# Performance work log

Hardware: AMD Instinct MI355X
Metric: run time of the kernel (lower is better)

The kernel has to match this reference:

```python
import jax, jax.numpy as jnp
import numpy as np


def conv2d(x, w, b=None):
    # NCHW conv, stride 1, 'same' padding inferred from kernel size
    ph, pw = w.shape[2] // 2, w.shape[3] // 2
    y = jax.lax.conv_general_dilated(
        x, w, window_strides=(1, 1), padding=[(ph, ph), (pw, pw)],
        dimension_numbers=('NCHW', 'OIHW', 'NCHW'))
    if b is not None:
        y = y + b[None, :, None, None]
    return y


def gelu(v):
    return jax.nn.gelu(v, approximate=False)  # torch nn.GELU default (erf)


def lrelu(v):
    return jnp.where(v >= 0, v, 0.1 * v)  # LeakyReLU(0.1)


def setup_inputs() -> dict:
    key = jax.random.key(0)
    ks = jax.random.split(key, 16)
    B, C, H, W = 2, 32, 256, 256
    s = 0.05
    return {
        'x':      jax.random.normal(ks[0], (B, C, H, W), jnp.float32),
        'key':    jax.random.normal(ks[1], (B, C, H, W), jnp.float32),
        'w_off1': jax.random.normal(ks[2], (32, 64, 3, 3), jnp.float32) * s,
        'b_off1': jax.random.normal(ks[3], (32,), jnp.float32) * s,
        'w_off2': jax.random.normal(ks[4], (32, 32, 3, 3), jnp.float32) * s,
        'b_off2': jax.random.normal(ks[5], (32,), jnp.float32) * s,
        'w_dcn':  jax.random.normal(ks[6], (288, 64, 3, 3), jnp.float32) * s,
        'b_dcn':  jax.random.normal(ks[7], (288,), jnp.float32) * s,
        'w_sel':  jax.random.normal(ks[8], (1, 3, 3, 3), jnp.float32) * s,
        'b_sel':  jax.random.normal(ks[9], (1,), jnp.float32) * s,
        'w_t1':   jax.random.normal(ks[10], (32, 32, 3, 3), jnp.float32) * s,
        'w_t2':   jax.random.normal(ks[11], (128, 32, 1, 1), jnp.float32) * s,
        'w_t3':   jax.random.normal(ks[12], (128, 128, 3, 3), jnp.float32) * s,
        'w_t4':   jax.random.normal(ks[13], (32, 128, 1, 1), jnp.float32) * s,
        'w_t5':   jax.random.normal(ks[14], (32, 32, 3, 3), jnp.float32) * s,
    }


def reference(x, key, w_off1, b_off1, w_off2, b_off2, w_dcn, b_dcn,
              w_sel, b_sel, w_t1, w_t2, w_t3, w_t4, w_t5):
    B, C, H, W = x.shape
    TOPK = 3
    # offset branch
    off = lrelu(conv2d(jnp.concatenate([x, key], axis=1), w_off1, b_off1))
    off = lrelu(conv2d(off, w_off2, b_off2))
    # dcn_attention proxy: conv over (key, offset) producing C*9 candidate warps
    warp = conv2d(jnp.concatenate([key, off], axis=1), w_dcn, b_dcn)
    warp = warp.reshape(B, C, 9, H, W)
    # correlation of each of 9 candidates with x, per pixel
    corr = jnp.einsum('bcohw,bchw->bohw', warp, x)            # [B,9,H,W]
    corr = corr.reshape(B, 9, H * W).transpose(0, 2, 1)       # [B,HW,9]
    _, idx = jax.lax.top_k(corr, TOPK)                        # [B,HW,3]
    # gather selected candidates per pixel per channel
    warp_p = warp.reshape(B, C, 9, H * W).transpose(0, 3, 2, 1)   # [B,HW,9,C]
    sel = jnp.take_along_axis(warp_p, idx[..., None], axis=2)     # [B,HW,3,C]
    key_warp = sel.reshape(B, H, W, TOPK, C).transpose(0, 4, 3, 1, 2)
    key_warp = key_warp.reshape(B * C, TOPK, H, W)
    key_warp = conv2d(key_warp, w_sel, b_sel).reshape(B, C, H, W)
    # tail: conv-GELU bottleneck stack
    y = conv2d(key_warp, w_t1)
    y = conv2d(gelu(y), w_t2)
    y = conv2d(gelu(y), w_t3)
    y = conv2d(gelu(y), w_t4)
    y = conv2d(gelu(y), w_t5)
    return y
```

## Files before the change

### kernel.cpp

```cpp
#include <hip/hip_runtime.h>
#include <math.h>

static constexpr int H = 256, W = 256, HW = H * W;

typedef __attribute__((ext_vector_type(8))) _Float16 half8v;
typedef __attribute__((ext_vector_type(4))) _Float16 half4v;
typedef __attribute__((ext_vector_type(4))) float  float4v;

__device__ __forceinline__ half8v h8zero() {
  half8v z;
  #pragma unroll
  for (int i = 0; i < 8; ++i) z[i] = (_Float16)0;
  return z;
}

__device__ __forceinline__ float gelu_f(float v) {
  return 0.5f * v * (1.0f + erff(v * 0.70710678118654752440f));
}
template<int ACT>
__device__ __forceinline__ float apply_act(float v) {
  if constexpr (ACT == 1) return v >= 0.f ? v : 0.1f * v;
  if constexpr (ACT == 2) return gelu_f(v);
  return v;
}

__global__ __launch_bounds__(256)
void pack2_k(const float* __restrict__ inA, _Float16* __restrict__ hiA, _Float16* __restrict__ loA,
             const float* __restrict__ inB, _Float16* __restrict__ hiB, _Float16* __restrict__ loB)
{
  const int p = blockIdx.x * 256 + threadIdx.x;
  const int b = blockIdx.y;
  const float* in = blockIdx.z ? inB : inA;
  _Float16* hi = blockIdx.z ? hiB : hiA;
  _Float16* lo = blockIdx.z ? loB : loA;
  const float* ip = in + (size_t)b * 32 * HW + p;
  __attribute__((aligned(16))) _Float16 hv[32], lv[32];
  #pragma unroll
  for (int c = 0; c < 32; ++c) {
    float v = ip[(size_t)c * HW];
    _Float16 h = (_Float16)v;
    hv[c] = h;
    lv[c] = (_Float16)((v - (float)h) * 2048.0f);
  }
  size_t ob = ((size_t)b * HW + p) * 32;
  #pragma unroll
  for (int j = 0; j < 4; ++j) {
    *(half8v*)&hi[ob + j * 8] = *(half8v*)&hv[j * 8];
    *(half8v*)&lo[ob + j * 8] = *(half8v*)&lv[j * 8];
  }
}

__device__ __forceinline__ void prep_w_body(const float* w, _Float16* hi, _Float16* lo,
                                            int OC, int CIN, int tid)
{
  if (tid >= OC * CIN * 9) return;
  int ci = tid % CIN; int r = tid / CIN; int oc = r % OC; int tap = r / OC;
  float v = w[((size_t)oc * CIN + ci) * 9 + tap];
  _Float16 h = (_Float16)v;
  hi[tid] = h;
  lo[tid] = (_Float16)((v - (float)h) * 2048.0f);
}
__global__ __launch_bounds__(256)
void prep3_w_k(const float* __restrict__ w0, _Float16* __restrict__ h0, _Float16* __restrict__ l0, int OC0, int CIN0, int nb0,
               const float* __restrict__ w1, _Float16* __restrict__ h1, _Float16* __restrict__ l1, int OC1, int CIN1, int nb1,
               const float* __restrict__ w2, _Float16* __restrict__ h2, _Float16* __restrict__ l2, int OC2, int CIN2)
{
  int bb = blockIdx.x;
  if (bb < nb0)            prep_w_body(w0, h0, l0, OC0, CIN0, bb * 256 + threadIdx.x);
  else if (bb < nb0 + nb1) prep_w_body(w1, h1, l1, OC1, CIN1, (bb - nb0) * 256 + threadIdx.x);
  else                     prep_w_body(w2, h2, l2, OC2, CIN2, (bb - nb0 - nb1) * 256 + threadIdx.x);
}

template<int CIN, int OC, int OCB, int ACT, int OMODE, int SPLIT>
__global__ __launch_bounds__(256)
void conv3x3_mfma_k(const _Float16* __restrict__ iH0, const _Float16* __restrict__ iL0,
                    const _Float16* __restrict__ iH1, const _Float16* __restrict__ iL1, int cin0,
                    const _Float16* __restrict__ wHi, const _Float16* __restrict__ wLo,
                    const float* __restrict__ bias,
                    float* __restrict__ outF, _Float16* __restrict__ oH, _Float16* __restrict__ oL)
{
  constexpr int NOF  = OCB / 16;
  constexpr int NAQ  = (SPLIT == 3) ? NOF : 1;
  constexpr int REC  = (SPLIT == 3) ? 64 : 32;
  constexpr int nOcg = OC / OCB;
  __shared__ _Float16 sB[6 * 66 * REC];

  const int l  = threadIdx.x & 63;
  const int wv = threadIdx.x >> 6;

  const int bid = blockIdx.x;
  const int xcd = bid & 7, q = bid >> 3;
  const int ocg  = q % nOcg;
  const int tIdx = (q / nOcg) * 8 + xcd;
  const int b   = tIdx >> 8;
  const int x0  = ((tIdx >> 6) & 3) * 64;
  const int y0  = (tIdx & 63) * 4;
  const int oc0 = ocg * OCB;

  float4v accP[NOF][4];
  float4v accQ[NAQ][4];
  #pragma unroll
  for (int j = 0; j < NOF; ++j)
    #pragma unroll
    for (int f = 0; f < 4; ++f)
      accP[j][f] = (float4v){0.f, 0.f, 0.f, 0.f};
  #pragma unroll
  for (int j = 0; j < NAQ; ++j)
    #pragma unroll
    for (int f = 0; f < 4; ++f)
      accQ[j][f] = (float4v){0.f, 0.f, 0.f, 0.f};

  const int k8  = (l >> 4) * 8;
  const int ocl = l & 15;
  const int rowy = y0 + wv;
  const int sq  = l & 3;
  const int spx = l >> 2;

  #pragma unroll 1
  for (int cc = 0; cc < CIN; cc += 32) {
    const _Float16 *cbH, *cbL;
    if (cc < cin0) {
      size_t o = (size_t)(b * (cin0 >> 5) + (cc >> 5)) * HW * 32;
      cbH = iH0 + o; cbL = iL0 + o;
    } else {
      size_t o = (size_t)(b * ((CIN - cin0) >> 5) + ((cc - cin0) >> 5)) * HW * 32;
      cbH = iH1 + o; cbL = iL1 + o;
    }
    __syncthreads();
    if constexpr (SPLIT == 3) {
      #pragma unroll 2
      for (int t = wv; t < 60; t += 4) {
        int r = t / 10; int rem = t - r * 10; int bsel = rem / 5; int s = rem - bsel * 5;
        const _Float16* src = bsel ? cbL : cbH;
        int gy = y0 + r - 1;
        bool vy = (gy >= 0) && (gy < H);
        int gyc = gy < 0 ? 0 : (gy >= H ? H - 1 : gy);
        int pxl = s * 16 + spx;
        bool lact = (s < 4) || (l < 8);
        int gx = x0 + pxl - 1;
        bool vx = (gx >= 0) && (gx < W);
        int gxc = gx < 0 ? 0 : (gx >= W ? W - 1 : gx);
        half8v v = h8zero();
        if (lact && vy && vx)
          v = *(const half8v*)&src[((size_t)gyc * W + gxc) * 32 + sq * 8];
        int cls = (sq + (bsel ? 4 : 0)) ^ (pxl & 7);
        if (lact)
          *(half8v*)&sB[(r * 66 + pxl) * 64 + cls * 8] = v;
      }
    } else {
      #pragma unroll 2
      for (int t = wv; t < 30; t += 4) {
        int r = t / 5; int s = t - r * 5;
        int gy = y0 + r - 1;
        bool vy = (gy >= 0) && (gy < H);
        int gyc = gy < 0 ? 0 : (gy >= H ? H - 1 : gy);
        int pxl = s * 16 + spx;
        bool lact = (s < 4) || (l < 8);
        int gx = x0 + pxl - 1;
        bool vx = (gx >= 0) && (gx < W);
        int gxc = gx < 0 ? 0 : (gx >= W ? W - 1 : gx);
        half8v v = h8zero();
        if (lact && vy && vx)
          v = *(const half8v*)&cbH[((size_t)gyc * W + gxc) * 32 + sq * 8];
        int cls = (sq ^ pxl) & 3;
        if (lact)
          *(half8v*)&sB[(r * 66 + pxl) * 32 + cls * 8] = v;
      }
    }
    __syncthreads();

    #pragma unroll 1
    for (int tap = 0; tap < 9; ++tap) {
      const int dy = tap / 3, dx = tap - 3 * (tap / 3);
      half8v ah[NOF], aq[NAQ];
      const _Float16* hp = wHi + ((size_t)tap * OC + oc0 + ocl) * CIN + cc + k8;
      #pragma unroll
      for (int j = 0; j < NOF; ++j)
        ah[j] = *(const half8v*)(hp + (size_t)j * 16 * CIN);
      if constexpr (SPLIT == 3) {
        const _Float16* lp = wLo + ((size_t)tap * OC + oc0 + ocl) * CIN + cc + k8;
        #pragma unroll
        for (int j = 0; j < NOF; ++j)
          aq[j] = *(const half8v*)(lp + (size_t)j * 16 * CIN);
      }
      const int px = ocl + dx;
      if constexpr (SPLIT == 3) {
        const int rbase = ((wv + dy) * 66 + px) * 64;
        const int clsH = (l >> 4) ^ (px & 7);
        const int clsQ = ((l >> 4) + 4) ^ (px & 7);
        __builtin_amdgcn_s_setprio(1);
        #pragma unroll
        for (int f = 0; f < 4; ++f) {
          half8v bh = *(const half8v*)&sB[rbase + f * 1024 + clsH * 8];
          half8v bq = *(const half8v*)&sB[rbase + f * 1024 + clsQ * 8];
          #pragma unroll
          for (int j = 0; j < NOF; ++j) {
            accP[j][f] = __builtin_amdgcn_mfma_f32_16x16x32_f16(ah[j], bh, accP[j][f], 0, 0, 0);
            accQ[j][f] = __builtin_amdgcn_mfma_f32_16x16x32_f16(ah[j], bq, accQ[j][f], 0, 0, 0);
            accQ[j][f] = __builtin_amdgcn_mfma_f32_16x16x32_f16(aq[j], bh, accQ[j][f], 0, 0, 0);
          }
        }
        __builtin_amdgcn_s_setprio(0);
      } else {
        const int rbase = ((wv + dy) * 66 + px) * 32;
        const int clsH = ((l >> 4) ^ px) & 3;
        __builtin_amdgcn_s_setprio(1);
        #pragma unroll
        for (int f = 0; f < 4; ++f) {
          half8v bh = *(const half8v*)&sB[rbase + f * 512 + clsH * 8];
          #pragma unroll
          for (int j = 0; j < NOF; ++j)
            accP[j][f] = __builtin_amdgcn_mfma_f32_16x16x32_f16(ah[j], bh, accP[j][f], 0, 0, 0);
        }
        __builtin_amdgcn_s_setprio(0);
      }
    }
  }

  #pragma unroll
  for (int j = 0; j < NOF; ++j)
    #pragma unroll
    for (int f = 0; f < 4; ++f) {
      const int px  = x0 + f * 16 + ocl;
      const int occ = oc0 + j * 16 + (l >> 4) * 4;
      float vv4[4];
      #pragma unroll
      for (int r = 0; r < 4; ++r) {
        float bv = bias ? bias[occ + r] : 0.f;
        float vv = accP[j][f][r] + bv;
        if constexpr (SPLIT == 3) vv += accQ[j][f][r] * (1.0f / 2048.0f);
        vv4[r] = apply_act<ACT>(vv);
      }
      if constexpr (OMODE == 0) {
        #pragma unroll
        for (int r = 0; r < 4; ++r)
          outF[((size_t)(b * OC + occ + r) * H + rowy) * W + px] = vv4[r];
      } else if constexpr (OMODE == 1) {
        __attribute__((aligned(8))) _Float16 hv[4], lv[4];
        #pragma unroll
        for (int r = 0; r < 4; ++r) {
          _Float16 h = (_Float16)vv4[r];
          hv[r] = h;
          lv[r] = (_Float16)((vv4[r] - (float)h) * 2048.0f);
        }
        size_t ob = ((size_t)b * HW + (size_t)rowy * W + px) * OC + occ;
        *(half4v*)&oH[ob] = *(half4v*)&hv[0];
        *(half4v*)&oL[ob] = *(half4v*)&lv[0];
      } else {
        __attribute__((aligned(8))) _Float16 hv[4];
        #pragma unroll
        for (int r = 0; r < 4; ++r) hv[r] = (_Float16)vv4[r];
        size_t ob = ((size_t)b * HW + (size_t)rowy * W + px) * OC + occ;
        *(half4v*)&oH[ob] = *(half4v*)&hv[0];
      }
    }
}

template<int CIN, int OCB, int ACT>
__global__ __launch_bounds__(256)
void conv1x1_nhwc_k(const _Float16* __restrict__ in, const float* __restrict__ w,
                    _Float16* __restrict__ oH, int OC)
{
  __shared__ __align__(16) float sW[OCB][CIN];
  const int b   = blockIdx.y;
  const int oc0 = blockIdx.z * OCB;
  for (int t = threadIdx.x; t < OCB * CIN; t += 256)
    sW[t / CIN][t % CIN] = w[(size_t)(oc0 + t / CIN) * CIN + (t % CIN)];
  __syncthreads();

  const int pb = blockIdx.x * 1024 + threadIdx.x;
  float acc[OCB][4];
  #pragma unroll
  for (int o = 0; o < OCB; ++o)
    #pragma unroll
    for (int i = 0; i < 4; ++i) acc[o][i] = 0.f;

  #pragma unroll 1
  for (int c0 = 0; c0 < CIN; c0 += 8) {
    float v[4][8];
    #pragma unroll
    for (int i = 0; i < 4; ++i) {
      const _Float16* ip = in + ((size_t)b * HW + pb + i * 256) * CIN + c0;
      half8v hv8 = *(const half8v*)ip;
      #pragma unroll
      for (int j = 0; j < 8; ++j) v[i][j] = (float)hv8[j];
    }
    #pragma unroll
    for (int o = 0; o < OCB; ++o) {
      const float4 w0 = *(const float4*)&sW[o][c0];
      const float4 w1 = *(const float4*)&sW[o][c0 + 4];
      #pragma unroll
      for (int i = 0; i < 4; ++i) {
        acc[o][i] += v[i][0]*w0.x + v[i][1]*w0.y + v[i][2]*w0.z + v[i][3]*w0.w
                   + v[i][4]*w1.x + v[i][5]*w1.y + v[i][6]*w1.z + v[i][7]*w1.w;
      }
    }
  }
  #pragma unroll
  for (int i = 0; i < 4; ++i) {
    __attribute__((aligned(16))) _Float16 hv[OCB];
    #pragma unroll
    for (int o = 0; o < OCB; ++o)
      hv[o] = (_Float16)apply_act<ACT>(acc[o][i]);
    size_t ob = ((size_t)(b * (OC >> 5) + (oc0 >> 5)) * HW + pb + i * 256) * 32 + (oc0 & 31);
    #pragma unroll
    for (int j = 0; j < OCB / 8; ++j)
      *(half8v*)&oH[ob + j * 8] = *(half8v*)&hv[j * 8];
  }
}

__global__ __launch_bounds__(256)
void corr_topk_k(const float* __restrict__ warp, const float* __restrict__ x,
                 int* __restrict__ idxo)
{
  const int p2 = (blockIdx.x * 256 + threadIdx.x) * 2;
  const int b = blockIdx.y;
  float corr[9][2];
  #pragma unroll
  for (int o = 0; o < 9; ++o) { corr[o][0] = 0.f; corr[o][1] = 0.f; }
  #pragma unroll 1
  for (int c = 0; c < 32; ++c) {
    float2 xv = *(const float2*)&x[((size_t)b * 32 + c) * HW + p2];
    const float* wp = warp + ((size_t)b * 288 + (size_t)c * 9) * HW + p2;
    #pragma unroll
    for (int o = 0; o < 9; ++o) {
      float2 wv = *(const float2*)&wp[(size_t)o * HW];
      corr[o][0] += wv.x * xv.x;
      corr[o][1] += wv.y * xv.y;
    }
  }
  int2 packs;
  #pragma unroll
  for (int i = 0; i < 2; ++i) {
    unsigned mask = 0;
    int packed = 0;
    #pragma unroll
    for (int t = 0; t < 3; ++t) {
      float best = -INFINITY; int bi = 0;
      #pragma unroll
      for (int o = 0; o < 9; ++o) {
        bool take = (((mask >> o) & 1u) == 0u) && (corr[o][i] > best);
        best = take ? corr[o][i] : best;
        bi   = take ? o          : bi;
      }
      mask   |= 1u << bi;
      packed |= bi << (4 * t);
    }
    ((int*)&packs)[i] = packed;
  }
  *(int2*)&idxo[(size_t)b * HW + p2] = packs;
}

__global__ __launch_bounds__(256)
void selconv_k(const float* __restrict__ warp, const int* __restrict__ idxp,
               const float* __restrict__ wsel, const float* __restrict__ bsel,
               _Float16* __restrict__ oH)
{
  const int tx = threadIdx.x & 31, ty = threadIdx.x >> 5;
  const int px = blockIdx.x * 32 + tx;
  const int py = blockIdx.y * 8 + ty;
  const int b  = blockIdx.z;

  int  nidx[9];
  bool nval[9];
  int  qoff[9];
  #pragma unroll
  for (int kh = 0; kh < 3; ++kh)
    #pragma unroll
    for (int kw = 0; kw < 3; ++kw) {
      int k = kh * 3 + kw;
      int qy = py + kh - 1, qx = px + kw - 1;
      nval[k] = (qy >= 0 && qy < H && qx >= 0 && qx < W);
      qoff[k] = qy * W + qx;
      nidx[k] = nval[k] ? idxp[(size_t)b * HW + qoff[k]] : 0;
    }

  float ws27[27];
  #pragma unroll
  for (int i = 0; i < 27; ++i) ws27[i] = wsel[i];
  const float bs = bsel[0];

  float arr[32];
  #pragma unroll 1
  for (int c = 0; c < 32; ++c) {
    float acc = bs;
    const float* wb = warp + ((size_t)b * 288 + (size_t)c * 9) * HW;
    #pragma unroll
    for (int k = 0; k < 9; ++k) {
      if (nval[k]) {
        int pk = nidx[k];
        #pragma unroll
        for (int t = 0; t < 3; ++t) {
          int o = (pk >> (4 * t)) & 15;
          acc += ws27[t * 9 + k] * wb[(size_t)o * HW + qoff[k]];
        }
      }
    }
    arr[c] = acc;
  }

  __attribute__((aligned(16))) _Float16 hv[32];
  #pragma unroll
  for (int c = 0; c < 32; ++c) hv[c] = (_Float16)arr[c];
  size_t ob = ((size_t)b * HW + (size_t)py * W + px) * 32;
  #pragma unroll
  for (int j = 0; j < 4; ++j)
    *(half8v*)&oH[ob + j * 8] = *(half8v*)&hv[j * 8];
}

extern "C" void kernel_launch(void* const* d_in, const int* in_sizes, int n_in,
                              void* d_out, int out_size, void* d_ws, size_t ws_size,
                              hipStream_t stream) {
  const float* x      = (const float*)d_in[0];
  const float* key    = (const float*)d_in[1];
  const float* w_off1 = (const float*)d_in[2];
  const float* b_off1 = (const float*)d_in[3];
  const float* w_off2 = (const float*)d_in[4];
  const float* b_off2 = (const float*)d_in[5];
  const float* w_dcn  = (const float*)d_in[6];
  const float* b_dcn  = (const float*)d_in[7];
  const float* w_sel  = (const float*)d_in[8];
  const float* b_sel  = (const float*)d_in[9];
  const float* w_t1   = (const float*)d_in[10];
  const float* w_t2   = (const float*)d_in[11];
  const float* w_t3   = (const float*)d_in[12];
  const float* w_t4   = (const float*)d_in[13];
  const float* w_t5   = (const float*)d_in[14];

  char* ws = (char*)d_ws;
  float* warp = (float*)(ws);
  _Float16* xH  = (_Float16*)(ws);
  _Float16* xL  = (_Float16*)(ws + 8388608);
  _Float16* o1H = (_Float16*)(ws + 16777216);
  _Float16* o1L = (_Float16*)(ws + 25165824);
  _Float16* w1H = (_Float16*)(ws + 33554432);
  _Float16* w1L = w1H + 18432;
  _Float16* w2H = w1L + 18432;
  _Float16* w2L = w2H + 9216;
  _Float16* kH  = (_Float16*)(ws + 150994944);
  _Float16* kL  = (_Float16*)(ws + 159383552);
  _Float16* o2H = (_Float16*)(ws + 167772160);
  _Float16* o2L = (_Float16*)(ws + 176160768);
  _Float16* wdH = (_Float16*)(ws + 184549376);
  _Float16* wdL = wdH + 165888;
  int*      idxb = (int*)(ws + 150994944);
  _Float16* kwH  = (_Float16*)(ws + 159383552);
  _Float16* twB  = (_Float16*)(ws + 176160768);
  _Float16* t1H_w = twB;
  _Float16* t1L_w = twB + 9216;
  _Float16* t3H_w = twB + 18432;
  _Float16* t3L_w = twB + 165888;
  _Float16* t5H_w = twB + 313344;
  _Float16* t5L_w = twB + 322560;
  _Float16* y1  = (_Float16*)(ws);
  _Float16* t2H = (_Float16*)(ws + 16777216);
  _Float16* y3  = (_Float16*)(ws + 83886080);
  _Float16* t4H = (_Float16*)(ws + 50331648);
  float* out = (float*)d_out;

  dim3 blk(256);

  pack2_k<<<dim3(256, 2, 2), blk, 0, stream>>>(x, xH, xL, key, kH, kL);
  prep3_w_k<<<dim3(756), blk, 0, stream>>>(
      w_off1, w1H, w1L, 32, 64, 72,
      w_off2, w2H, w2L, 32, 32, 36,
      w_dcn,  wdH, wdL, 288, 64);

  conv3x3_mfma_k<64, 32, 32, 1, 1, 3><<<dim3(512), blk, 0, stream>>>(
      xH, xL, kH, kL, 32, w1H, w1L, b_off1, nullptr, o1H, o1L);
  conv3x3_mfma_k<32, 32, 32, 1, 1, 3><<<dim3(512), blk, 0, stream>>>(
      o1H, o1L, o1H, o1L, 32, w2H, w2L, b_off2, nullptr, o2H, o2L);
  conv3x3_mfma_k<64, 288, 32, 0, 0, 3><<<dim3(4608), blk, 0, stream>>>(
      kH, kL, o2H, o2L, 32, wdH, wdL, b_dcn, warp, nullptr, nullptr);
  corr_topk_k<<<dim3(128, 2), blk, 0, stream>>>(warp, x, idxb);
  selconv_k<<<dim3(8, 32, 2), blk, 0, stream>>>(warp, idxb, w_sel, b_sel, kwH);

  prep3_w_k<<<dim3(648), blk, 0, stream>>>(
      w_t1, t1H_w, t1L_w, 32, 32, 36,
      w_t3, t3H_w, t3L_w, 128, 128, 576,
      w_t5, t5H_w, t5L_w, 32, 32);

  conv3x3_mfma_k<32, 32, 32, 2, 3, 1><<<dim3(512), blk, 0, stream>>>(
      kwH, kwH, kwH, kwH, 32, t1H_w, t1L_w, nullptr, nullptr, y1, nullptr);
  conv1x1_nhwc_k<32, 16, 2><<<dim3(64, 2, 8), blk, 0, stream>>>(y1, w_t2, t2H, 128);
  conv3x3_mfma_k<128, 128, 64, 2, 3, 1><<<dim3(1024), blk, 0, stream>>>(
      t2H, t2H, t2H, t2H, 128, t3H_w, t3L_w, nullptr, nullptr, y3, nullptr);
  conv1x1_nhwc_k<128, 16, 2><<<dim3(64, 2, 2), blk, 0, stream>>>(y3, w_t4, t4H, 32);
  conv3x3_mfma_k<32, 32, 32, 0, 0, 1><<<dim3(512), blk, 0, stream>>>(
      t4H, t4H, t4H, t4H, 32, t5H_w, t5L_w, nullptr, out, nullptr, nullptr);
}
```

Before: 646.7 us.

## Use zero-padded interleaved hi/lo NHWC layout with direct global-to-LDS loads

Stores the hi and lo fp16 halves of the split-precision activations interleaved in one 64-channel record per pixel, in a 258x258 buffer whose zero border is written by a new kernel. The SPLIT==3 conv tile loader then drops all bounds checks and clamping and uses global_load_lds to copy 16-byte chunks straight into shared memory with a pre-swizzled source address. The goal is to cut address arithmetic, register staging and divergent boundary handling in the three offset/DCN convs. In exchange it adds a border-zeroing launch, enlarges the buffers, and reshuffles workspace offsets, so any aliasing mistake could corrupt data.

```diff
diff --git a/kernel.cpp b/kernel.cpp
--- a/kernel.cpp
+++ b/kernel.cpp
@@ -2,6 +2,7 @@
 #include <math.h>
 
 static constexpr int H = 256, W = 256, HW = H * W;
+static constexpr int PW = 258, PREC = 66564;
 
 typedef __attribute__((ext_vector_type(8))) _Float16 half8v;
 typedef __attribute__((ext_vector_type(4))) _Float16 half4v;
@@ -12,6 +13,12 @@
   #pragma unroll
   for (int i = 0; i < 8; ++i) z[i] = (_Float16)0;
   return z;
+}
+
+__device__ __forceinline__ void gload_lds16(const _Float16* g, _Float16* lds) {
+  __builtin_amdgcn_global_load_lds(
+      (const __attribute__((address_space(1))) void*)g,
+      (__attribute__((address_space(3))) void*)lds, 16, 0, 0);
 }
 
 __device__ __forceinline__ float gelu_f(float v) {
@@ -25,14 +32,32 @@
 }
 
 __global__ __launch_bounds__(256)
-void pack2_k(const float* __restrict__ inA, _Float16* __restrict__ hiA, _Float16* __restrict__ loA,
-             const float* __restrict__ inB, _Float16* __restrict__ hiB, _Float16* __restrict__ loB)
+void zero_border_k(_Float16* p0, _Float16* p1, _Float16* p2, _Float16* p3)
+{
+  int t = blockIdx.x * 256 + threadIdx.x;
+  if (t >= 1028) return;
+  int inst = blockIdx.y;
+  _Float16* P = (inst >> 1) == 0 ? p0 : ((inst >> 1) == 1 ? p1 : ((inst >> 1) == 2 ? p2 : p3));
+  int b = inst & 1;
+  int y, x;
+  if      (t < 258) { y = 0;          x = t; }
+  else if (t < 516) { y = 257;        x = t - 258; }
+  else if (t < 772) { y = t - 515;    x = 0; }
+  else              { y = t - 771;    x = 257; }
+  _Float16* o = P + (((size_t)b * PW + y) * PW + x) * 64;
+  half8v z = h8zero();
+  #pragma unroll
+  for (int j = 0; j < 8; ++j) *(half8v*)&o[j * 8] = z;
+}
+
+__global__ __launch_bounds__(256)
+void pack2_k(const float* __restrict__ inA, _Float16* __restrict__ pA,
+             const float* __restrict__ inB, _Float16* __restrict__ pB)
 {
   const int p = blockIdx.x * 256 + threadIdx.x;
   const int b = blockIdx.y;
   const float* in = blockIdx.z ? inB : inA;
-  _Float16* hi = blockIdx.z ? hiB : hiA;
-  _Float16* lo = blockIdx.z ? loB : loA;
+  _Float16* P = blockIdx.z ? pB : pA;
   const float* ip = in + (size_t)b * 32 * HW + p;
   __attribute__((aligned(16))) _Float16 hv[32], lv[32];
   #pragma unroll
@@ -42,11 +67,12 @@
     hv[c] = h;
     lv[c] = (_Float16)((v - (float)h) * 2048.0f);
   }
-  size_t ob = ((size_t)b * HW + p) * 32;
+  const int y = p >> 8, xcol = p & 255;
+  _Float16* o = P + (((size_t)b * PW + y + 1) * PW + xcol + 1) * 64;
   #pragma unroll
   for (int j = 0; j < 4; ++j) {
-    *(half8v*)&hi[ob + j * 8] = *(half8v*)&hv[j * 8];
-    *(half8v*)&lo[ob + j * 8] = *(half8v*)&lv[j * 8];
+    *(half8v*)&o[j * 8]      = *(half8v*)&hv[j * 8];
+    *(half8v*)&o[32 + j * 8] = *(half8v*)&lv[j * 8];
   }
 }
 
@@ -118,36 +144,37 @@
 
   #pragma unroll 1
   for (int cc = 0; cc < CIN; cc += 32) {
-    const _Float16 *cbH, *cbL;
-    if (cc < cin0) {
-      size_t o = (size_t)(b * (cin0 >> 5) + (cc >> 5)) * HW * 32;
-      cbH = iH0 + o; cbL = iL0 + o;
+    if constexpr (SPLIT == 3) {
+      const _Float16* cb = (cc < cin0 ? iH0 : iH1) + (size_t)b * ((size_t)PREC * 64);
+      __syncthreads();
+      #pragma unroll
+      for (int k = 0; k < 12; ++k) {
+        int t = wv + 4 * k;
+        int r = t >> 3, s = t & 7;
+        const _Float16* src = cb
+            + (((size_t)(y0 + r) * PW) + (x0 + s * 8 + (l >> 3))) * 64
+            + ((l & 7) ^ (l >> 3)) * 8;
+        gload_lds16(src, &sB[(r * 66 + s * 8) * 64]);
+      }
+      #pragma unroll
+      for (int rr = wv; rr < 6; rr += 4) {
+        if (l < 16) {
+          int pxo = l >> 3;
+          int slot = l & 7;
+          const _Float16* src = cb
+              + (((size_t)(y0 + rr) * PW) + (x0 + 64 + pxo)) * 64 + (slot ^ pxo) * 8;
+          half8v v = *(const half8v*)src;
+          *(half8v*)&sB[(rr * 66 + 64 + pxo) * 64 + slot * 8] = v;
+        }
+      }
+      __syncthreads();
     } else {
-      size_t o = (size_t)(b * ((CIN - cin0) >> 5) + ((cc - cin0) >> 5)) * HW * 32;
-      cbH = iH1 + o; cbL = iL1 + o;
-    }
-    __syncthreads();
-    if constexpr (SPLIT == 3) {
-      #pragma unroll 2
-      for (int t = wv; t < 60; t += 4) {
-        int r = t / 10; int rem = t - r * 10; int bsel = rem / 5; int s = rem - bsel * 5;
-        const _Float16* src = bsel ? cbL : cbH;
-        int gy = y0 + r - 1;
-        bool vy = (gy >= 0) && (gy < H);
-        int gyc = gy < 0 ? 0 : (gy >= H ? H - 1 : gy);
-        int pxl = s * 16 + spx;
-        bool lact = (s < 4) || (l < 8);
-        int gx = x0 + pxl - 1;
-        bool vx = (gx >= 0) && (gx < W);
-        int gxc = gx < 0 ? 0 : (gx >= W ? W - 1 : gx);
-        half8v v = h8zero();
-        if (lact && vy && vx)
-          v = *(const half8v*)&src[((size_t)gyc * W + gxc) * 32 + sq * 8];
-        int cls = (sq + (bsel ? 4 : 0)) ^ (pxl & 7);
-        if (lact)
-          *(half8v*)&sB[(r * 66 + pxl) * 64 + cls * 8] = v;
-      }
-    } else {
+      const _Float16* cbH;
+      {
+        size_t o = (size_t)(b * (CIN >> 5) + (cc >> 5)) * HW * 32;
+        cbH = iH0 + o;
+      }
+      __syncthreads();
       #pragma unroll 2
       for (int t = wv; t < 30; t += 4) {
         int r = t / 5; int s = t - r * 5;
@@ -166,8 +193,8 @@
         if (lact)
           *(half8v*)&sB[(r * 66 + pxl) * 32 + cls * 8] = v;
       }
-    }
-    __syncthreads();
+      __syncthreads();
+    }
 
     #pragma unroll 1
     for (int tap = 0; tap < 9; ++tap) {
@@ -243,9 +270,9 @@
           hv[r] = h;
           lv[r] = (_Float16)((vv4[r] - (float)h) * 2048.0f);
         }
-        size_t ob = ((size_t)b * HW + (size_t)rowy * W + px) * OC + occ;
-        *(half4v*)&oH[ob] = *(half4v*)&hv[0];
-        *(half4v*)&oL[ob] = *(half4v*)&lv[0];
+        size_t rec = ((size_t)b * PW + rowy + 1) * PW + px + 1;
+        *(half4v*)&oH[rec * 64 + occ]      = *(half4v*)&hv[0];
+        *(half4v*)&oH[rec * 64 + 32 + occ] = *(half4v*)&lv[0];
       } else {
         __attribute__((aligned(8))) _Float16 hv[4];
         #pragma unroll
@@ -429,23 +456,19 @@
 
   char* ws = (char*)d_ws;
   float* warp = (float*)(ws);
-  _Float16* xH  = (_Float16*)(ws);
-  _Float16* xL  = (_Float16*)(ws + 8388608);
-  _Float16* o1H = (_Float16*)(ws + 16777216);
-  _Float16* o1L = (_Float16*)(ws + 25165824);
-  _Float16* w1H = (_Float16*)(ws + 33554432);
-  _Float16* w1L = w1H + 18432;
-  _Float16* w2H = w1L + 18432;
-  _Float16* w2L = w2H + 9216;
-  _Float16* kH  = (_Float16*)(ws + 150994944);
-  _Float16* kL  = (_Float16*)(ws + 159383552);
-  _Float16* o2H = (_Float16*)(ws + 167772160);
-  _Float16* o2L = (_Float16*)(ws + 176160768);
-  _Float16* wdH = (_Float16*)(ws + 184549376);
-  _Float16* wdL = wdH + 165888;
+  _Float16* xP   = (_Float16*)(ws);
+  _Float16* o1P  = (_Float16*)(ws + 17040384);
+  _Float16* w1H  = (_Float16*)(ws + 34080768);
+  _Float16* w1L  = w1H + 18432;
+  _Float16* w2H  = w1L + 18432;
+  _Float16* w2L  = w2H + 9216;
+  _Float16* wdH  = (_Float16*)(ws + 150994944);
+  _Float16* wdL  = wdH + 165888;
+  _Float16* keyP = (_Float16*)(ws + 151658496);
+  _Float16* o2P  = (_Float16*)(ws + 168698880);
   int*      idxb = (int*)(ws + 150994944);
-  _Float16* kwH  = (_Float16*)(ws + 159383552);
-  _Float16* twB  = (_Float16*)(ws + 176160768);
+  _Float16* kwH  = (_Float16*)(ws + 151658496);
+  _Float16* twB  = (_Float16*)(ws + 160047104);
   _Float16* t1H_w = twB;
   _Float16* t1L_w = twB + 9216;
   _Float16* t3H_w = twB + 18432;
@@ -454,24 +477,25 @@
   _Float16* t5L_w = twB + 322560;
   _Float16* y1  = (_Float16*)(ws);
   _Float16* t2H = (_Float16*)(ws + 16777216);
+  _Float16* t4H = (_Float16*)(ws + 50331648);
   _Float16* y3  = (_Float16*)(ws + 83886080);
-  _Float16* t4H = (_Float16*)(ws + 50331648);
   float* out = (float*)d_out;
 
   dim3 blk(256);
 
-  pack2_k<<<dim3(256, 2, 2), blk, 0, stream>>>(x, xH, xL, key, kH, kL);
+  zero_border_k<<<dim3(5, 8), blk, 0, stream>>>(xP, keyP, o1P, o2P);
+  pack2_k<<<dim3(256, 2, 2), blk, 0, stream>>>(x, xP, key, keyP);
   prep3_w_k<<<dim3(756), blk, 0, stream>>>(
       w_off1, w1H, w1L, 32, 64, 72,
       w_off2, w2H, w2L, 32, 32, 36,
       w_dcn,  wdH, wdL, 288, 64);
 
   conv3x3_mfma_k<64, 32, 32, 1, 1, 3><<<dim3(512), blk, 0, stream>>>(
-      xH, xL, kH, kL, 32, w1H, w1L, b_off1, nullptr, o1H, o1L);
+      xP, nullptr, keyP, nullptr, 32, w1H, w1L, b_off1, nullptr, o1P, nullptr);
   conv3x3_mfma_k<32, 32, 32, 1, 1, 3><<<dim3(512), blk, 0, stream>>>(
-      o1H, o1L, o1H, o1L, 32, w2H, w2L, b_off2, nullptr, o2H, o2L);
+      o1P, nullptr, nullptr, nullptr, 32, w2H, w2L, b_off2, nullptr, o2P, nullptr);
   conv3x3_mfma_k<64, 288, 32, 0, 0, 3><<<dim3(4608), blk, 0, stream>>>(
-      kH, kL, o2H, o2L, 32, wdH, wdL, b_dcn, warp, nullptr, nullptr);
+      keyP, nullptr, o2P, nullptr, 32, wdH, wdL, b_dcn, warp, nullptr, nullptr);
   corr_topk_k<<<dim3(128, 2), blk, 0, stream>>>(warp, x, idxb);
   selconv_k<<<dim3(8, 32, 2), blk, 0, stream>>>(warp, idxb, w_sel, b_sel, kwH);
 
@@ -481,11 +505,11 @@
       w_t5, t5H_w, t5L_w, 32, 32);
 
   conv3x3_mfma_k<32, 32, 32, 2, 3, 1><<<dim3(512), blk, 0, stream>>>(
-      kwH, kwH, kwH, kwH, 32, t1H_w, t1L_w, nullptr, nullptr, y1, nullptr);
+      kwH, nullptr, nullptr, nullptr, 32, t1H_w, t1L_w, nullptr, nullptr, y1, nullptr);
   conv1x1_nhwc_k<32, 16, 2><<<dim3(64, 2, 8), blk, 0, stream>>>(y1, w_t2, t2H, 128);
   conv3x3_mfma_k<128, 128, 64, 2, 3, 1><<<dim3(1024), blk, 0, stream>>>(
-      t2H, t2H, t2H, t2H, 128, t3H_w, t3L_w, nullptr, nullptr, y3, nullptr);
+      t2H, nullptr, nullptr, nullptr, 128, t3H_w, t3L_w, nullptr, nullptr, y3, nullptr);
   conv1x1_nhwc_k<128, 16, 2><<<dim3(64, 2, 2), blk, 0, stream>>>(y3, w_t4, t4H, 32);
   conv3x3_mfma_k<32, 32, 32, 0, 0, 1><<<dim3(512), blk, 0, stream>>>(
-      t4H, t4H, t4H, t4H, 32, t5H_w, t5L_w, nullptr, out, nullptr, nullptr);
-}
+      t4H, nullptr, nullptr, nullptr, 32, t5H_w, t5L_w, nullptr, out, nullptr, nullptr);
+}
```

After: 606.0 us. 6.3% less time.
